# Kernel optimization log

Measured on AMD Instinct MI355X. Metric: run time of the kernel, lower is better.

## Reference

```python
import jax, jax.numpy as jnp
import numpy as np

GRID = 32
GBOUND = 0.5
GRID_MIN = -GBOUND + GBOUND / GRID  # as in point2voxel


def _voxel_index(points):
    # points: [B,N,3] -> linear voxel indices [B,N]
    vx = (points - GRID_MIN) * GRID / (2.0 * GBOUND)
    vx = jnp.round(jnp.clip(vx, 0.0, GRID - 1))
    lin = vx @ jnp.array([GRID * GRID, GRID, 1], dtype=vx.dtype)
    return lin.astype(jnp.int32)


def _distance_loss(points, cps, v):
    # points [B,N,3], cps [B,G^3,3], v [B,G^3]
    lin = _voxel_index(points)                               # [B,N]
    mask = 1.0 - jnp.take_along_axis(v, lin, axis=1)         # [B,N]
    idx3 = jnp.broadcast_to(lin[:, :, None], lin.shape + (3,))
    gathered = jnp.take_along_axis(cps, idx3, axis=1)        # [B,N,3]
    d = (points - gathered) * mask[:, :, None]
    n2 = jnp.sum(d * d, axis=2)
    norm = jnp.sqrt(jnp.maximum(n2, 1e-30))                  # safe L2 norm
    return jnp.mean(jnp.sum(norm, axis=1))


def _plane_point(p, plane):
    # p [B,N,3], plane [B,1,4] -> reflected points [B,N,3]
    length = 2.0 * (jnp.sum(p * plane[..., :3], axis=2, keepdims=True) + plane[..., 3:4])
    norm2 = jnp.sum(plane[..., :3] ** 2, axis=2, keepdims=True)
    return p - length * plane[..., :3] / (norm2 + 1e-8)


def _quat_mul(q1, q2):
    w1, x1, y1, z1 = q1[..., 0], q1[..., 1], q1[..., 2], q1[..., 3]
    w2, x2, y2, z2 = q2[..., 0], q2[..., 1], q2[..., 2], q2[..., 3]
    w = w1 * w2 - x1 * x2 - y1 * y2 - z1 * z2
    x = w1 * x2 + x1 * w2 + y1 * z2 - z1 * y2
    y = w1 * y2 - x1 * z2 + y1 * w2 + z1 * x2
    z = w1 * z2 + x1 * y2 - y1 * x2 + z1 * w2
    return jnp.stack([w, x, y, z], axis=-1)


def _rotate_point(p, q):
    # p [B,N,3], q [B,1,4]
    B, N, _ = p.shape
    pq = jnp.concatenate([jnp.zeros((B, N, 1), p.dtype), p], axis=-1)
    qc = q * jnp.array([1.0, -1.0, -1.0, -1.0], q.dtype)
    return _quat_mul(_quat_mul(q, pq), qc)[..., 1:]


def setup_inputs() -> dict:
    key = jax.random.key(0)
    k = jax.random.split(key, 5)
    S, B, N, G = 3, 512, 1000, 32
    return {
        "planes": jax.random.normal(k[0], (S, B, 4), dtype=jnp.float32),
        "quats": jax.random.normal(k[1], (S, B, 4), dtype=jnp.float32),
        "closestPoints": jax.random.normal(k[2], (B, G ** 3 * 3), dtype=jnp.float32),
        "surfaceSamples": jax.random.normal(k[3], (B, N, 3), dtype=jnp.float32),
        "volume": jax.random.uniform(k[4], (B, 1, G, G, G), dtype=jnp.float32),
    }


def reference(planes, quats, closestPoints, surfaceSamples, volume):
    B = volume.shape[0]
    v = volume.reshape(B, GRID ** 3)
    cps = closestPoints.reshape(B, -1, 3)

    def per_sym(plane, quat):
        pl = plane[:, None, :]  # [B,1,4]
        lp = _distance_loss(_plane_point(surfaceSamples, pl), cps, v)
        qt = quat[:, None, :]
        lq = _distance_loss(_rotate_point(surfaceSamples, qt), cps, v)
        return lp, lq

    lps, lqs = jax.vmap(per_sym)(planes, quats)  # vectorized over S symmetry elems
    # sum over S then / S == mean, matching the torch loop
    return jnp.mean(lps), jnp.mean(lqs)
```

## Files before the change

### kernel.cpp

```cpp
#include <hip/hip_runtime.h>
#include <math.h>


#define NGRID3     32768
#define GRID_MIN_F (-0.484375f)
#define NTHREADS   256

__device__ __forceinline__ float point_loss(float x, float y, float z,
                                            const float* __restrict__ vol,
                                            const float* __restrict__ cp)
{
    float fx = fminf(fmaxf((x - GRID_MIN_F) * 32.0f, 0.0f), 31.0f);
    float fy = fminf(fmaxf((y - GRID_MIN_F) * 32.0f, 0.0f), 31.0f);
    float fz = fminf(fmaxf((z - GRID_MIN_F) * 32.0f, 0.0f), 31.0f);
    int lin = ((int)rintf(fx)) * 1024 + ((int)rintf(fy)) * 32 + (int)rintf(fz);

    float m  = 1.0f - vol[lin];
    int  c3  = lin * 3;
    float dx = (x - cp[c3 + 0]) * m;
    float dy = (y - cp[c3 + 1]) * m;
    float dz = (z - cp[c3 + 2]) * m;
    return sqrtf(fmaxf(dx * dx + dy * dy + dz * dz, 1e-30f));
}

template <int S>
__global__ __launch_bounds__(NTHREADS, 4) void symloss_stage1(
    const float* __restrict__ planes,
    const float* __restrict__ quats,
    const float* __restrict__ cps,
    const float* __restrict__ samples,
    const float* __restrict__ volume,
    float* __restrict__ partials,
    int B, int N)
{
    const int bid = blockIdx.x;
    const int b   = bid % B;
    const int c   = bid / B;

    const float* __restrict__ vol = volume + (size_t)b * NGRID3;
    const float* __restrict__ cp  = cps    + (size_t)b * NGRID3 * 3;

    float plx[S], ply[S], plz[S], plw[S], inv_n2[S];
    float qw[S], qx[S], qy[S], qz[S], w2mu[S];
#pragma unroll
    for (int s = 0; s < S; ++s) {
        float4 pl = ((const float4*)planes)[(size_t)s * B + b];
        float4 q  = ((const float4*)quats )[(size_t)s * B + b];
        plx[s] = pl.x; ply[s] = pl.y; plz[s] = pl.z; plw[s] = pl.w;
        inv_n2[s] = 1.0f / (pl.x * pl.x + pl.y * pl.y + pl.z * pl.z + 1e-8f);
        qw[s] = q.x; qx[s] = q.y; qy[s] = q.z; qz[s] = q.w;
        w2mu[s] = q.x * q.x - (q.y * q.y + q.z * q.z + q.w * q.w);
    }

    float sum_p = 0.0f, sum_q = 0.0f;
    const int n = c * NTHREADS + (int)threadIdx.x;
    if (n < N) {
        const float* sp = samples + ((size_t)b * N + n) * 3;
        const float px = sp[0];
        const float py = sp[1];
        const float pz = sp[2];
#pragma unroll
        for (int s = 0; s < S; ++s) {
            float f = 2.0f * (px * plx[s] + py * ply[s] + pz * plz[s] + plw[s]) * inv_n2[s];
            sum_p += point_loss(px - f * plx[s], py - f * ply[s], pz - f * plz[s], vol, cp);

            float udp = qx[s] * px + qy[s] * py + qz[s] * pz;
            float cx  = qy[s] * pz - qz[s] * py;
            float cy  = qz[s] * px - qx[s] * pz;
            float cz  = qx[s] * py - qy[s] * px;
            sum_q += point_loss(w2mu[s] * px + 2.0f * (udp * qx[s] + qw[s] * cx),
                                w2mu[s] * py + 2.0f * (udp * qy[s] + qw[s] * cy),
                                w2mu[s] * pz + 2.0f * (udp * qz[s] + qw[s] * cz),
                                vol, cp);
        }
    }

    for (int off = 32; off > 0; off >>= 1) {
        sum_p += __shfl_down(sum_p, off);
        sum_q += __shfl_down(sum_q, off);
    }
    __shared__ float red[NTHREADS / 64][2];
    const int lane = threadIdx.x & 63;
    const int wid  = threadIdx.x >> 6;
    if (lane == 0) { red[wid][0] = sum_p; red[wid][1] = sum_q; }
    __syncthreads();

    if (threadIdx.x == 0) {
        float tp = 0.0f, tq = 0.0f;
        for (int w = 0; w < NTHREADS / 64; ++w) { tp += red[w][0]; tq += red[w][1]; }
        partials[2 * bid + 0] = tp;
        partials[2 * bid + 1] = tq;
    }
}

__global__ __launch_bounds__(NTHREADS) void symloss_reduce(
    const float* __restrict__ partials, int M, float scale,
    float* __restrict__ out)
{
    double sp = 0.0, sq = 0.0;
    for (int i = threadIdx.x; i < M; i += NTHREADS) {
        sp += (double)partials[2 * i + 0];
        sq += (double)partials[2 * i + 1];
    }
    for (int off = 32; off > 0; off >>= 1) {
        sp += __shfl_down(sp, off);
        sq += __shfl_down(sq, off);
    }
    __shared__ double red[NTHREADS / 64][2];
    const int lane = threadIdx.x & 63;
    const int wid  = threadIdx.x >> 6;
    if (lane == 0) { red[wid][0] = sp; red[wid][1] = sq; }
    __syncthreads();
    if (threadIdx.x == 0) {
        double tp = 0.0, tq = 0.0;
        for (int w = 0; w < NTHREADS / 64; ++w) { tp += red[w][0]; tq += red[w][1]; }
        out[0] = (float)(tp * (double)scale);
        out[1] = (float)(tq * (double)scale);
    }
}

extern "C" void kernel_launch(void* const* d_in, const int* in_sizes, int n_in,
                              void* d_out, int out_size, void* d_ws, size_t ws_size,
                              hipStream_t stream)
{
    const float* planes  = (const float*)d_in[0];
    const float* quats   = (const float*)d_in[1];
    const float* cps     = (const float*)d_in[2];
    const float* samples = (const float*)d_in[3];
    const float* volume  = (const float*)d_in[4];
    float* out = (float*)d_out;

    const int B = in_sizes[4] / NGRID3;
    const int S = in_sizes[0] / (B * 4);
    const int N = in_sizes[3] / (B * 3);
    const int C = (N + NTHREADS - 1) / NTHREADS;
    const float scale = 1.0f / (float)(S * B);

    float* partials = (float*)d_ws;
    int M = C * B;

    switch (S) {
    case 1: symloss_stage1<1><<<C * B, NTHREADS, 0, stream>>>(planes, quats, cps, samples, volume, partials, B, N); break;
    case 2: symloss_stage1<2><<<C * B, NTHREADS, 0, stream>>>(planes, quats, cps, samples, volume, partials, B, N); break;
    case 3: symloss_stage1<3><<<C * B, NTHREADS, 0, stream>>>(planes, quats, cps, samples, volume, partials, B, N); break;
    case 4: symloss_stage1<4><<<C * B, NTHREADS, 0, stream>>>(planes, quats, cps, samples, volume, partials, B, N); break;
    default:
        for (int s = 0; s < S; ++s)
            symloss_stage1<1><<<C * B, NTHREADS, 0, stream>>>(
                planes + (size_t)s * B * 4, quats + (size_t)s * B * 4,
                cps, samples, volume, partials + (size_t)s * C * B * 2, B, N);
        M = S * C * B;
        break;
    }

    symloss_reduce<<<1, NTHREADS, 0, stream>>>(partials, M, scale, out);
}
```

Measured before the change: 302.0 us.

## Flatten point/symmetry work items and remap blocks to XCDs per batch

```diff
diff --git a/kernel.cpp b/kernel.cpp
--- a/kernel.cpp
+++ b/kernel.cpp
@@ -4,7 +4,8 @@
 
 #define NGRID3     32768
 #define GRID_MIN_F (-0.484375f)
-#define NTHREADS   256
+#define T1         512
+#define T2         256
 
 __device__ __forceinline__ float point_loss(float x, float y, float z,
                                             const float* __restrict__ vol,
@@ -24,53 +25,63 @@
 }
 
 template <int S>
-__global__ __launch_bounds__(NTHREADS, 4) void symloss_stage1(
+__global__ __launch_bounds__(T1, 4) void symloss_stage1(
     const float* __restrict__ planes,
     const float* __restrict__ quats,
     const float* __restrict__ cps,
     const float* __restrict__ samples,
     const float* __restrict__ volume,
     float* __restrict__ partials,
-    int B, int N)
+    int B, int N, int C, int xcd_map)
 {
     const int bid = blockIdx.x;
-    const int b   = bid % B;
-    const int c   = bid / B;
+    int b, c;
+    if (xcd_map) {
+        const int x = bid & 7;
+        const int g = bid >> 3;
+        c = g % C;
+        b = (g / C) * 8 + x;
+    } else {
+        b = bid / C;
+        c = bid % C;
+    }
 
     const float* __restrict__ vol = volume + (size_t)b * NGRID3;
     const float* __restrict__ cp  = cps    + (size_t)b * NGRID3 * 3;
+    const float* __restrict__ sp  = samples + (size_t)b * N * 3;
 
-    float plx[S], ply[S], plz[S], plw[S], inv_n2[S];
-    float qw[S], qx[S], qy[S], qz[S], w2mu[S];
-#pragma unroll
-    for (int s = 0; s < S; ++s) {
-        float4 pl = ((const float4*)planes)[(size_t)s * B + b];
-        float4 q  = ((const float4*)quats )[(size_t)s * B + b];
-        plx[s] = pl.x; ply[s] = pl.y; plz[s] = pl.z; plw[s] = pl.w;
-        inv_n2[s] = 1.0f / (pl.x * pl.x + pl.y * pl.y + pl.z * pl.z + 1e-8f);
-        qw[s] = q.x; qx[s] = q.y; qy[s] = q.z; qz[s] = q.w;
-        w2mu[s] = q.x * q.x - (q.y * q.y + q.z * q.z + q.w * q.w);
-    }
+    const int items  = N * 2 * S;
+    const int stride = C * T1;
+    const int tib    = c * T1 + (int)threadIdx.x;
 
     float sum_p = 0.0f, sum_q = 0.0f;
-    const int n = c * NTHREADS + (int)threadIdx.x;
-    if (n < N) {
-        const float* sp = samples + ((size_t)b * N + n) * 3;
-        const float px = sp[0];
-        const float py = sp[1];
-        const float pz = sp[2];
-#pragma unroll
-        for (int s = 0; s < S; ++s) {
-            float f = 2.0f * (px * plx[s] + py * ply[s] + pz * plz[s] + plw[s]) * inv_n2[s];
-            sum_p += point_loss(px - f * plx[s], py - f * ply[s], pz - f * plz[s], vol, cp);
 
-            float udp = qx[s] * px + qy[s] * py + qz[s] * pz;
-            float cx  = qy[s] * pz - qz[s] * py;
-            float cy  = qz[s] * px - qx[s] * pz;
-            float cz  = qx[s] * py - qy[s] * px;
-            sum_q += point_loss(w2mu[s] * px + 2.0f * (udp * qx[s] + qw[s] * cx),
-                                w2mu[s] * py + 2.0f * (udp * qy[s] + qw[s] * cy),
-                                w2mu[s] * pz + 2.0f * (udp * qz[s] + qw[s] * cz),
+    for (int e = tib; e < items; e += stride) {
+        const bool is_q = (e >= N * S);
+        const int idx   = is_q ? (e - N * S) : e;
+        const int n     = idx / S;
+        const int s     = idx - n * S;
+
+        const float px = sp[n * 3 + 0];
+        const float py = sp[n * 3 + 1];
+        const float pz = sp[n * 3 + 2];
+
+        if (!is_q) {
+            const float4 pl = ((const float4*)planes)[(size_t)s * B + b];
+            const float inv_n2 = 1.0f / (pl.x * pl.x + pl.y * pl.y + pl.z * pl.z + 1e-8f);
+            const float f = 2.0f * (px * pl.x + py * pl.y + pz * pl.z + pl.w) * inv_n2;
+            sum_p += point_loss(px - f * pl.x, py - f * pl.y, pz - f * pl.z, vol, cp);
+        } else {
+            const float4 q = ((const float4*)quats)[(size_t)s * B + b];
+            const float qw = q.x, qx = q.y, qy = q.z, qz = q.w;
+            const float w2mu = qw * qw - (qx * qx + qy * qy + qz * qz);
+            const float udp = qx * px + qy * py + qz * pz;
+            const float cx  = qy * pz - qz * py;
+            const float cy  = qz * px - qx * pz;
+            const float cz  = qx * py - qy * px;
+            sum_q += point_loss(w2mu * px + 2.0f * (udp * qx + qw * cx),
+                                w2mu * py + 2.0f * (udp * qy + qw * cy),
+                                w2mu * pz + 2.0f * (udp * qz + qw * cz),
                                 vol, cp);
         }
     }
@@ -79,7 +90,7 @@
         sum_p += __shfl_down(sum_p, off);
         sum_q += __shfl_down(sum_q, off);
     }
-    __shared__ float red[NTHREADS / 64][2];
+    __shared__ float red[T1 / 64][2];
     const int lane = threadIdx.x & 63;
     const int wid  = threadIdx.x >> 6;
     if (lane == 0) { red[wid][0] = sum_p; red[wid][1] = sum_q; }
@@ -87,18 +98,18 @@
 
     if (threadIdx.x == 0) {
         float tp = 0.0f, tq = 0.0f;
-        for (int w = 0; w < NTHREADS / 64; ++w) { tp += red[w][0]; tq += red[w][1]; }
+        for (int w = 0; w < T1 / 64; ++w) { tp += red[w][0]; tq += red[w][1]; }
         partials[2 * bid + 0] = tp;
         partials[2 * bid + 1] = tq;
     }
 }
 
-__global__ __launch_bounds__(NTHREADS) void symloss_reduce(
+__global__ __launch_bounds__(T2) void symloss_reduce(
     const float* __restrict__ partials, int M, float scale,
     float* __restrict__ out)
 {
     double sp = 0.0, sq = 0.0;
-    for (int i = threadIdx.x; i < M; i += NTHREADS) {
+    for (int i = threadIdx.x; i < M; i += T2) {
         sp += (double)partials[2 * i + 0];
         sq += (double)partials[2 * i + 1];
     }
@@ -106,14 +117,14 @@
         sp += __shfl_down(sp, off);
         sq += __shfl_down(sq, off);
     }
-    __shared__ double red[NTHREADS / 64][2];
+    __shared__ double red[T2 / 64][2];
     const int lane = threadIdx.x & 63;
     const int wid  = threadIdx.x >> 6;
     if (lane == 0) { red[wid][0] = sp; red[wid][1] = sq; }
     __syncthreads();
     if (threadIdx.x == 0) {
         double tp = 0.0, tq = 0.0;
-        for (int w = 0; w < NTHREADS / 64; ++w) { tp += red[w][0]; tq += red[w][1]; }
+        for (int w = 0; w < T2 / 64; ++w) { tp += red[w][0]; tq += red[w][1]; }
         out[0] = (float)(tp * (double)scale);
         out[1] = (float)(tq * (double)scale);
     }
@@ -133,25 +144,30 @@
     const int B = in_sizes[4] / NGRID3;
     const int S = in_sizes[0] / (B * 4);
     const int N = in_sizes[3] / (B * 3);
-    const int C = (N + NTHREADS - 1) / NTHREADS;
     const float scale = 1.0f / (float)(S * B);
 
+    const int items = N * 2 * S;
+    int C = (items + 2 * T1 - 1) / (2 * T1);
+    if (C < 8) C = 8;
+    const int xcd_map = (B % 8 == 0) ? 1 : 0;
+
     float* partials = (float*)d_ws;
-    int M = C * B;
+    int M = B * C;
 
     switch (S) {
-    case 1: symloss_stage1<1><<<C * B, NTHREADS, 0, stream>>>(planes, quats, cps, samples, volume, partials, B, N); break;
-    case 2: symloss_stage1<2><<<C * B, NTHREADS, 0, stream>>>(planes, quats, cps, samples, volume, partials, B, N); break;
-    case 3: symloss_stage1<3><<<C * B, NTHREADS, 0, stream>>>(planes, quats, cps, samples, volume, partials, B, N); break;
-    case 4: symloss_stage1<4><<<C * B, NTHREADS, 0, stream>>>(planes, quats, cps, samples, volume, partials, B, N); break;
+    case 1: symloss_stage1<1><<<B * C, T1, 0, stream>>>(planes, quats, cps, samples, volume, partials, B, N, C, xcd_map); break;
+    case 2: symloss_stage1<2><<<B * C, T1, 0, stream>>>(planes, quats, cps, samples, volume, partials, B, N, C, xcd_map); break;
+    case 3: symloss_stage1<3><<<B * C, T1, 0, stream>>>(planes, quats, cps, samples, volume, partials, B, N, C, xcd_map); break;
+    case 4: symloss_stage1<4><<<B * C, T1, 0, stream>>>(planes, quats, cps, samples, volume, partials, B, N, C, xcd_map); break;
     default:
         for (int s = 0; s < S; ++s)
-            symloss_stage1<1><<<C * B, NTHREADS, 0, stream>>>(
+            symloss_stage1<1><<<B * C, T1, 0, stream>>>(
                 planes + (size_t)s * B * 4, quats + (size_t)s * B * 4,
-                cps, samples, volume, partials + (size_t)s * C * B * 2, B, N);
-        M = S * C * B;
+                cps, samples, volume, partials + (size_t)s * B * C * 2,
+                B, N, C, xcd_map);
+        M = S * B * C;
         break;
     }
 
-    symloss_reduce<<<1, NTHREADS, 0, stream>>>(partials, M, scale, out);
+    symloss_reduce<<<1, T2, 0, stream>>>(partials, M, scale, out);
 }
```

Result: no change. 300.9 us (-0.4%).
